# Performance work log

Measured on AMD Instinct MI355X. Metric: run time of the kernel, lower is better.

The kernel has to match this reference:

```python
import jax, jax.numpy as jnp
import numpy as np


def setup_inputs() -> dict:
    key = jax.random.key(0)
    k1, k2 = jax.random.split(key)
    B, L = 8192, 4096
    v = jax.random.normal(k1, (B, L), dtype=jnp.float32)
    z = jax.random.normal(k2, (B, L), dtype=jnp.float32)
    return {"v": v, "z": z}


def reference(v, z):
    # Householder reflection: z_new = z - 2 * v (v . z) / ||v||^2
    # Mathematically identical to the original bmm(v v^T, z) formulation,
    # but contracts the rank-1 outer product analytically (no BxLxL tensor).
    vz = jnp.sum(v * z, axis=1, keepdims=True)        # [B, 1] = v . z per row
    norm_sq = jnp.sum(v * v, axis=1, keepdims=True)    # [B, 1] = ||v||^2
    return z - 2.0 * v * (vz / norm_sq)
```

## Files before the change

kernel.cpp:

```cpp
#include <hip/hip_runtime.h>
#include <hip/hip_bf16.h>


#define L_DIM 4096
#define BLOCK 256
#define VEC (L_DIM / 4)
#define PER_THREAD (VEC / BLOCK)

__global__ __launch_bounds__(BLOCK) void householder_kernel(
    const float* __restrict__ v,
    const float* __restrict__ z,
    float* __restrict__ out)
{
    __shared__ float s_red[2][4];

    const int row = blockIdx.x;
    const size_t base = (size_t)row * L_DIM;
    const float4* v4 = (const float4*)(v + base);
    const float4* z4 = (const float4*)(z + base);
    float4* o4 = (float4*)(out + base);

    float4 a[PER_THREAD];
    float4 b[PER_THREAD];

    #pragma unroll
    for (int k = 0; k < PER_THREAD; ++k) {
        const int i = threadIdx.x + k * BLOCK;
        a[k] = v4[i];
        b[k] = z4[i];
    }

    float vz = 0.0f, vv = 0.0f;
    #pragma unroll
    for (int k = 0; k < PER_THREAD; ++k) {
        vz = fmaf(a[k].x, b[k].x, vz); vz = fmaf(a[k].y, b[k].y, vz);
        vz = fmaf(a[k].z, b[k].z, vz); vz = fmaf(a[k].w, b[k].w, vz);
        vv = fmaf(a[k].x, a[k].x, vv); vv = fmaf(a[k].y, a[k].y, vv);
        vv = fmaf(a[k].z, a[k].z, vv); vv = fmaf(a[k].w, a[k].w, vv);
    }

    #pragma unroll
    for (int off = 32; off > 0; off >>= 1) {
        vz += __shfl_down(vz, off, 64);
        vv += __shfl_down(vv, off, 64);
    }

    const int wave = threadIdx.x >> 6;
    const int lane = threadIdx.x & 63;
    if (lane == 0) {
        s_red[0][wave] = vz;
        s_red[1][wave] = vv;
    }
    __syncthreads();

    const float tvz = s_red[0][0] + s_red[0][1] + s_red[0][2] + s_red[0][3];
    const float tvv = s_red[1][0] + s_red[1][1] + s_red[1][2] + s_red[1][3];
    const float s = -2.0f * tvz / tvv;

    #pragma unroll
    for (int k = 0; k < PER_THREAD; ++k) {
        const int i = threadIdx.x + k * BLOCK;
        float4 r;
        r.x = fmaf(s, a[k].x, b[k].x);
        r.y = fmaf(s, a[k].y, b[k].y);
        r.z = fmaf(s, a[k].z, b[k].z);
        r.w = fmaf(s, a[k].w, b[k].w);
        o4[i] = r;
    }
}

extern "C" void kernel_launch(void* const* d_in, const int* in_sizes, int n_in,
                              void* d_out, int out_size, void* d_ws, size_t ws_size,
                              hipStream_t stream) {
    const float* v = (const float*)d_in[0];
    const float* z = (const float*)d_in[1];
    float* out = (float*)d_out;
    const int B = in_sizes[0] / L_DIM;
    householder_kernel<<<B, BLOCK, 0, stream>>>(v, z, out);
}
```

Measured before the change: 307.6 us.

## Map one row per wavefront and drop block-level shared-memory reduction

Each 64-lane wave now processes a full row, with four rows per block, so the row reduction finishes using only xor-shuffles and needs no shared memory or __syncthreads. This removes the block barrier and LDS traffic and gives each lane more outstanding loads. In exchange, each lane holds 32 float4 values in registers, which raises VGPR pressure and may lower occupancy.

Measured after the change: 306.9 us. Within noise of the previous version (-0.3%).

```diff
diff --git a/kernel.cpp b/kernel.cpp
--- a/kernel.cpp
+++ b/kernel.cpp
@@ -4,35 +4,36 @@
 
 #define L_DIM 4096
 #define BLOCK 256
-#define VEC (L_DIM / 4)
-#define PER_THREAD (VEC / BLOCK)
+#define ROWS_PER_BLOCK 4
+#define F4_PER_LANE (L_DIM / 4 / 64)
 
 __global__ __launch_bounds__(BLOCK) void householder_kernel(
     const float* __restrict__ v,
     const float* __restrict__ z,
     float* __restrict__ out)
 {
-    __shared__ float s_red[2][4];
+    const int wave = threadIdx.x >> 6;
+    const int lane = threadIdx.x & 63;
+    const int row  = blockIdx.x * ROWS_PER_BLOCK + wave;
 
-    const int row = blockIdx.x;
     const size_t base = (size_t)row * L_DIM;
     const float4* v4 = (const float4*)(v + base);
     const float4* z4 = (const float4*)(z + base);
     float4* o4 = (float4*)(out + base);
 
-    float4 a[PER_THREAD];
-    float4 b[PER_THREAD];
+    float4 a[F4_PER_LANE];
+    float4 b[F4_PER_LANE];
 
     #pragma unroll
-    for (int k = 0; k < PER_THREAD; ++k) {
-        const int i = threadIdx.x + k * BLOCK;
+    for (int k = 0; k < F4_PER_LANE; ++k) {
+        const int i = lane + 64 * k;
         a[k] = v4[i];
         b[k] = z4[i];
     }
 
     float vz = 0.0f, vv = 0.0f;
     #pragma unroll
-    for (int k = 0; k < PER_THREAD; ++k) {
+    for (int k = 0; k < F4_PER_LANE; ++k) {
         vz = fmaf(a[k].x, b[k].x, vz); vz = fmaf(a[k].y, b[k].y, vz);
         vz = fmaf(a[k].z, b[k].z, vz); vz = fmaf(a[k].w, b[k].w, vz);
         vv = fmaf(a[k].x, a[k].x, vv); vv = fmaf(a[k].y, a[k].y, vv);
@@ -41,25 +42,15 @@
 
     #pragma unroll
     for (int off = 32; off > 0; off >>= 1) {
-        vz += __shfl_down(vz, off, 64);
-        vv += __shfl_down(vv, off, 64);
+        vz += __shfl_xor(vz, off, 64);
+        vv += __shfl_xor(vv, off, 64);
     }
 
-    const int wave = threadIdx.x >> 6;
-    const int lane = threadIdx.x & 63;
-    if (lane == 0) {
-        s_red[0][wave] = vz;
-        s_red[1][wave] = vv;
-    }
-    __syncthreads();
-
-    const float tvz = s_red[0][0] + s_red[0][1] + s_red[0][2] + s_red[0][3];
-    const float tvv = s_red[1][0] + s_red[1][1] + s_red[1][2] + s_red[1][3];
-    const float s = -2.0f * tvz / tvv;
+    const float s = -2.0f * vz / vv;
 
     #pragma unroll
-    for (int k = 0; k < PER_THREAD; ++k) {
-        const int i = threadIdx.x + k * BLOCK;
+    for (int k = 0; k < F4_PER_LANE; ++k) {
+        const int i = lane + 64 * k;
         float4 r;
         r.x = fmaf(s, a[k].x, b[k].x);
         r.y = fmaf(s, a[k].y, b[k].y);
@@ -76,5 +67,6 @@
     const float* z = (const float*)d_in[1];
     float* out = (float*)d_out;
     const int B = in_sizes[0] / L_DIM;
-    householder_kernel<<<B, BLOCK, 0, stream>>>(v, z, out);
+    const int grid = B / ROWS_PER_BLOCK;
+    householder_kernel<<<grid, BLOCK, 0, stream>>>(v, z, out);
 }
```
